# Performance work log

Measured on AMD Instinct MI355X. Metric: run time of the kernel, lower is better.

The kernel has to match this reference:

```python
import jax, jax.numpy as jnp
import numpy as np

B, N, F, H, C, HID = 2, 2048, 64, 4, 32, 128
HIN = H * C  # 128, GAT output width (concat heads)


def setup_inputs() -> dict:
    key = jax.random.key(0)
    ks = jax.random.split(key, 16)
    glorot = jax.nn.initializers.glorot_normal()
    x = jax.random.normal(ks[0], (B, N, F), jnp.float32)
    a = (jax.random.uniform(ks[1], (B, N, N)) < 0.01).astype(jnp.float32)
    a = jnp.maximum(a, jnp.eye(N, dtype=jnp.float32)[None])
    h = jax.random.normal(ks[2], (B, N, HID), jnp.float32)
    # GATConv params (spektral batch mode, concat_heads=True)
    kernel = glorot(ks[3], (F, H, C), jnp.float32)
    attn_self = glorot(ks[4], (H, C), jnp.float32)
    attn_nei = glorot(ks[5], (H, C), jnp.float32)
    bias_gat = jnp.zeros((HIN,), jnp.float32)
    # GRU-style gate params
    b_u = glorot(ks[6], (N, 1), jnp.float32)
    b_r = glorot(ks[7], (N, 1), jnp.float32)
    b_c = glorot(ks[8], (N, 1), jnp.float32)
    W_u = glorot(ks[9], (HID + HIN, HID), jnp.float32)
    W_r = glorot(ks[10], (HID + HIN, HID), jnp.float32)
    W_c = glorot(ks[11], (HID + HIN, HID), jnp.float32)
    # bilinear decoder (p) weight
    R_p = glorot(ks[12], (HID, HID), jnp.float32)
    return {"x": x, "a": a, "h": h, "kernel": kernel, "attn_self": attn_self,
            "attn_nei": attn_nei, "bias_gat": bias_gat, "b_u": b_u, "b_r": b_r,
            "b_c": b_c, "W_u": W_u, "W_r": W_r, "W_c": W_c, "R_p": R_p}


def _gat(x, a, kernel, attn_self, attn_nei, bias_gat):
    # x: [B,N,F] -> per-head features xp: [B,N,H,C]
    xp = jnp.einsum('bnf,fhc->bnhc', x, kernel)
    es = jnp.einsum('bnhc,hc->bnh', xp, attn_self)   # target score
    en = jnp.einsum('bnhc,hc->bnh', xp, attn_nei)    # source score
    # e[b,i,j,h] = leakyrelu(es_i + en_j), masked by adjacency
    e = jax.nn.leaky_relu(es[:, :, None, :] + en[:, None, :, :], 0.2)
    e = e + (-1e9) * (1.0 - a)[..., None]
    alpha = jax.nn.softmax(e, axis=2)                # softmax over sources j
    out = jnp.einsum('bijh,bjhc->bihc', alpha, xp)   # aggregate
    return out.reshape(out.shape[0], out.shape[1], -1) + bias_gat  # [B,N,H*C]


def reference(x, a, h, kernel, attn_self, attn_nei, bias_gat,
              b_u, b_r, b_c, W_u, W_r, W_c, R_p):
    conv_u = _gat(x, a, kernel, attn_self, attn_nei, bias_gat)  # [B,N,HIN]
    z = jnp.concatenate([conv_u, h], axis=-1)                    # [B,N,HIN+HID]
    u = jax.nn.sigmoid(b_u + z @ W_u)                            # b_u [N,1] broadcasts
    r = jax.nn.sigmoid(b_r + z @ W_r)
    zc = jnp.concatenate([conv_u, r * h], axis=-1)
    c = jnp.tanh(b_c + zc @ W_c)
    h_prime = u * h + (1.0 - u) * c                              # [B,N,HID]
    A = jnp.einsum('bnh,hk,bmk->bnm', h_prime, R_p, h_prime)     # bilinear decode [B,N,N]
    return A, h_prime
```

## Files before the change

kernel.cpp:

```cpp
#include <hip/hip_runtime.h>
#include <hip/hip_bf16.h>
#include <math.h>

#define NB 2
#define NN 2048
#define FD 64
#define NH 4
#define HIDD 128
#define ROWS_TOT (NB*NN)

#define XP_OFF   0
#define ES_OFF   524288
#define EN_OFF   540672
#define CU_OFF   557056
#define TBF_OFF  1081344
#define HPBF_OFF 1343488
#define WUH_OFF  1605632
#define WUL_OFF  1622016
#define WRH_OFF  1638400
#define WRL_OFF  1654784
#define WCH_OFF  1671168
#define WCL_OFF  1687552
#define RPH_OFF  1703936
#define RPL_OFF  1712128

#define A_ELEMS (NB*NN*NN)

typedef __attribute__((ext_vector_type(8))) short bf16x8;
typedef __attribute__((ext_vector_type(8))) unsigned short ushort8;
typedef __attribute__((ext_vector_type(4))) unsigned short ushort4v;
typedef __attribute__((ext_vector_type(4))) float f32x4;

#define MFMA_BF16(a,b,c) __builtin_amdgcn_mfma_f32_16x16x32_bf16((a),(b),(c),0,0,0)

static __device__ inline unsigned short f2bf(float x) {
  __hip_bfloat16 b = __float2bfloat16(x);
  unsigned short u; __builtin_memcpy(&u, &b, 2); return u;
}
static __device__ inline float bf2f(unsigned short u) {
  __hip_bfloat16 b; __builtin_memcpy(&b, &u, 2); return __bfloat162float(b);
}
static __device__ inline void split2(float x, unsigned short& hi, unsigned short& lo) {
  hi = f2bf(x);
  lo = f2bf(x - bf2f(hi));
}

__global__ __launch_bounds__(256) void k0_prep(
    const float* __restrict__ Wu, const float* __restrict__ Wr,
    const float* __restrict__ Wc, const float* __restrict__ Rp,
    unsigned short* __restrict__ wuh, unsigned short* __restrict__ wul,
    unsigned short* __restrict__ wrh, unsigned short* __restrict__ wrl,
    unsigned short* __restrict__ wch, unsigned short* __restrict__ wcl,
    unsigned short* __restrict__ rph, unsigned short* __restrict__ rpl)
{
  const int gid = blockIdx.x*256 + threadIdx.x;
  if (gid < 98304) {
    const int which = gid >> 15;
    const int loc = gid & 32767;
    const int e  = loc & 7;
    const int ln = (loc >> 3) & 63;
    const int ks = (loc >> 9) & 7;
    const int jt = loc >> 12;
    const int j = jt*16 + (ln & 15);
    const int k = ks*32 + ((ln >> 4) << 3) + e;
    const float* W = which == 0 ? Wu : (which == 1 ? Wr : Wc);
    unsigned short* oh = which == 0 ? wuh : (which == 1 ? wrh : wch);
    unsigned short* ol = which == 0 ? wul : (which == 1 ? wrl : wcl);
    unsigned short h, l; split2(W[k*128 + j], h, l);
    oh[loc] = h; ol[loc] = l;
  } else if (gid < 114688) {
    const int loc = gid - 98304;
    const int e  = loc & 7;
    const int ln = (loc >> 3) & 63;
    const int ks = (loc >> 9) & 3;
    const int jt = loc >> 11;
    const int j = jt*16 + (ln & 15);
    const int k = ks*32 + ((ln >> 4) << 3) + e;
    unsigned short h, l; split2(Rp[k*128 + j], h, l);
    rph[loc] = h; rpl[loc] = l;
  }
}

__global__ __launch_bounds__(256) void k1_xp(
    const float* __restrict__ x, const float* __restrict__ kern,
    const float* __restrict__ as_, const float* __restrict__ an_,
    float* __restrict__ xp, float* __restrict__ es, float* __restrict__ en)
{
  __shared__ float xr[8][FD];
  const int t = threadIdx.x;
  const int row0 = blockIdx.x * 8;
  for (int idx = t; idx < 8*FD; idx += 256)
    xr[idx >> 6][idx & 63] = x[(size_t)row0*FD + idx];
  __syncthreads();
  const int c4 = (t & 31) * 4;
  const int rq = t >> 5;
  const float4 asv = *(const float4*)(as_ + c4);
  const float4 anv = *(const float4*)(an_ + c4);
  float4 acc = make_float4(0.f, 0.f, 0.f, 0.f);
  for (int f = 0; f < FD; ++f) {
    const float4 kv = *(const float4*)(kern + f*128 + c4);
    const float xv = xr[rq][f];
    acc.x = fmaf(xv, kv.x, acc.x);
    acc.y = fmaf(xv, kv.y, acc.y);
    acc.z = fmaf(xv, kv.z, acc.z);
    acc.w = fmaf(xv, kv.w, acc.w);
  }
  const int grow = row0 + rq;
  *(float4*)(xp + (size_t)grow*128 + c4) = acc;
  float s  = acc.x*asv.x + acc.y*asv.y + acc.z*asv.z + acc.w*asv.w;
  float n_ = acc.x*anv.x + acc.y*anv.y + acc.z*anv.z + acc.w*anv.w;
#pragma unroll
  for (int mk = 4; mk >= 1; mk >>= 1) {
    s  += __shfl_xor(s,  mk, 64);
    n_ += __shfl_xor(n_, mk, 64);
  }
  if ((t & 7) == 0) {
    const int h = (t & 31) >> 3;
    es[grow*NH + h] = s; en[grow*NH + h] = n_;
  }
}

__global__ __launch_bounds__(256) void k2_attn(
    const float* __restrict__ a, const float* __restrict__ xp,
    const float* __restrict__ es, const float* __restrict__ en,
    const float* __restrict__ bias, float* __restrict__ cu)
{
  __shared__ unsigned short sidx[4][NN];
  __shared__ float swl[4][64][NH];
  const int t = threadIdx.x;
  const int ln = t & 63, wv = t >> 6;
  const int row = blockIdx.x * 4 + wv;
  const int b = row >> 11;
  const float4 esi = *(const float4*)(es + (size_t)row*NH);

  int deg = 0;
  const float4* arow4 = (const float4*)(a + (size_t)row*NN);
#pragma unroll
  for (int cch = 0; cch < 8; ++cch) {
    const float4 v = arow4[cch*64 + ln];
    const int j0 = cch*256 + ln*4;
    const float vv[4] = {v.x, v.y, v.z, v.w};
#pragma unroll
    for (int q = 0; q < 4; ++q) {
      const unsigned long long m = __ballot(vv[q] > 0.5f);
      if (vv[q] > 0.5f) {
        const int pos = deg + (int)__popcll(m & ((1ull << ln) - 1ull));
        sidx[wv][pos] = (unsigned short)(j0 + q);
      }
      deg += (int)__popcll(m);
    }
  }

  const int col0 = ln, col1 = ln + 64;
  const int h0 = ln >> 5;
  float m0=-1e30f, m1=-1e30f, m2=-1e30f, m3=-1e30f;
  float s0=0.f, s1=0.f, s2=0.f, s3=0.f;
  float acc0=0.f, acc1=0.f;
  for (int base = 0; base < deg; base += 64) {
    const int rem = min(64, deg - base);
    float t0=-1e30f, t1=-1e30f, t2=-1e30f, t3=-1e30f;
    if (ln < rem) {
      const int j = sidx[wv][base + ln];
      const float4 e4 = *(const float4*)(en + (size_t)(b*NN + j)*NH);
      t0 = esi.x + e4.x; t0 = t0 > 0.f ? t0 : 0.2f*t0;
      t1 = esi.y + e4.y; t1 = t1 > 0.f ? t1 : 0.2f*t1;
      t2 = esi.z + e4.z; t2 = t2 > 0.f ? t2 : 0.2f*t2;
      t3 = esi.w + e4.w; t3 = t3 > 0.f ? t3 : 0.2f*t3;
    }
    float c0=t0, c1=t1, c2=t2, c3=t3;
#pragma unroll
    for (int mk = 32; mk >= 1; mk >>= 1) {
      c0 = fmaxf(c0, __shfl_xor(c0, mk));
      c1 = fmaxf(c1, __shfl_xor(c1, mk));
      c2 = fmaxf(c2, __shfl_xor(c2, mk));
      c3 = fmaxf(c3, __shfl_xor(c3, mk));
    }
    const float nm0 = fmaxf(m0,c0), nm1 = fmaxf(m1,c1);
    const float nm2 = fmaxf(m2,c2), nm3 = fmaxf(m3,c3);
    const float r0 = expf(m0-nm0), r1 = expf(m1-nm1);
    const float r2 = expf(m2-nm2), r3 = expf(m3-nm3);
    s0 *= r0; s1 *= r1; s2 *= r2; s3 *= r3;
    float w0=0.f, w1=0.f, w2=0.f, w3=0.f;
    if (ln < rem) {
      w0 = expf(t0-nm0); w1 = expf(t1-nm1);
      w2 = expf(t2-nm2); w3 = expf(t3-nm3);
    }
    float u0=w0, u1=w1, u2=w2, u3=w3;
#pragma unroll
    for (int mk = 32; mk >= 1; mk >>= 1) {
      u0 += __shfl_xor(u0, mk);
      u1 += __shfl_xor(u1, mk);
      u2 += __shfl_xor(u2, mk);
      u3 += __shfl_xor(u3, mk);
    }
    s0 += u0; s1 += u1; s2 += u2; s3 += u3;
    acc0 *= (h0 ? r1 : r0);
    acc1 *= (h0 ? r3 : r2);
    swl[wv][ln][0] = w0; swl[wv][ln][1] = w1;
    swl[wv][ln][2] = w2; swl[wv][ln][3] = w3;
#pragma unroll 4
    for (int k = 0; k < rem; ++k) {
      const int j = sidx[wv][base + k];
      const float* xr = xp + (size_t)(b*NN + j)*128;
      acc0 = fmaf(swl[wv][k][h0],     xr[col0], acc0);
      acc1 = fmaf(swl[wv][k][2 + h0], xr[col1], acc1);
    }
    m0=nm0; m1=nm1; m2=nm2; m3=nm3;
  }
  const float den0 = h0 ? s1 : s0;
  const float den1 = h0 ? s3 : s2;
  cu[(size_t)row*128 + col0] = acc0/den0 + bias[col0];
  cu[(size_t)row*128 + col1] = acc1/den1 + bias[col1];
}

__global__ __launch_bounds__(512) void k3_mfma(
    const float* __restrict__ cu_, const float* __restrict__ hin,
    const float* __restrict__ bu, const float* __restrict__ br,
    const float* __restrict__ bc,
    const unsigned short* __restrict__ wuh, const unsigned short* __restrict__ wul,
    const unsigned short* __restrict__ wrh, const unsigned short* __restrict__ wrl,
    const unsigned short* __restrict__ wch, const unsigned short* __restrict__ wcl,
    const unsigned short* __restrict__ rph, const unsigned short* __restrict__ rpl,
    float* __restrict__ hp_out,
    __hip_bfloat16* __restrict__ hp_bf, __hip_bfloat16* __restrict__ t_bf)
{
  __shared__ __align__(16) char zH[16*512];
  __shared__ __align__(16) char zL[16*512];
  __shared__ __align__(16) char rhH[16*256];
  __shared__ __align__(16) char rhL[16*256];
  __shared__ __align__(16) char hpH[16*256];
  __shared__ __align__(16) char hpLo[16*256];
  const int t = threadIdx.x;
  const int row0 = blockIdx.x * 16;

#pragma unroll
  for (int i = 0; i < 2; ++i) {
    const int q = t + 512*i;
    const int r = q >> 6;
    const int c = (q & 63) * 4;
    float4 v;
    if (c < 128) v = *(const float4*)(cu_ + (size_t)(row0+r)*128 + c);
    else         v = *(const float4*)(hin + (size_t)(row0+r)*128 + (c-128));
    unsigned short hx, lx, hy, ly, hz, lz, hw, lw;
    split2(v.x, hx, lx); split2(v.y, hy, ly);
    split2(v.z, hz, lz); split2(v.w, hw, lw);
    ushort4v h4; h4[0]=hx; h4[1]=hy; h4[2]=hz; h4[3]=hw;
    ushort4v l4; l4[0]=lx; l4[1]=ly; l4[2]=lz; l4[3]=lw;
    const int byte = (c*2) ^ ((r & 7) << 4);
    *(ushort4v*)(zH + r*512 + byte) = h4;
    *(ushort4v*)(zL + r*512 + byte) = l4;
  }
  __syncthreads();

  const int ln = t & 63, wv = t >> 6;
  const int lr = ln & 15, kid = ln >> 4;
  const int sw = (lr & 7) << 4;
  const int colg = wv*16 + lr;
  const f32x4 zero = {0.f, 0.f, 0.f, 0.f};
  const bf16x8* wuhF = (const bf16x8*)wuh;
  const bf16x8* wulF = (const bf16x8*)wul;
  const bf16x8* wrhF = (const bf16x8*)wrh;
  const bf16x8* wrlF = (const bf16x8*)wrl;
  const bf16x8* wchF = (const bf16x8*)wch;
  const bf16x8* wclF = (const bf16x8*)wcl;
  const bf16x8* rphF = (const bf16x8*)rph;
  const bf16x8* rplF = (const bf16x8*)rpl;

  f32x4 accU = zero, accR = zero;
#pragma unroll
  for (int ks = 0; ks < 8; ++ks) {
    const int kb = ks*64 + kid*16;
    const bf16x8 ah = *(const bf16x8*)(zH + lr*512 + (kb ^ sw));
    const bf16x8 al = *(const bf16x8*)(zL + lr*512 + (kb ^ sw));
    const int fb = (wv*8 + ks)*64 + ln;
    const bf16x8 buH = wuhF[fb];
    const bf16x8 buL = wulF[fb];
    const bf16x8 brH = wrhF[fb];
    const bf16x8 brL = wrlF[fb];
    accU = MFMA_BF16(ah, buH, accU);
    accU = MFMA_BF16(ah, buL, accU);
    accU = MFMA_BF16(al, buH, accU);
    accR = MFMA_BF16(ah, brH, accR);
    accR = MFMA_BF16(ah, brL, accR);
    accR = MFMA_BF16(al, brH, accR);
  }

  float hval[4], uval[4];
#pragma unroll
  for (int reg = 0; reg < 4; ++reg) {
    const int row16 = kid*4 + reg;
    const int grow = row0 + row16;
    const int nrow = grow & (NN-1);
    const float h_ = hin[(size_t)grow*128 + colg];
    const float uv = 1.f/(1.f + expf(-(bu[nrow] + accU[reg])));
    const float rv = 1.f/(1.f + expf(-(br[nrow] + accR[reg])));
    hval[reg] = h_; uval[reg] = uv;
    unsigned short hs, ls; split2(rv * h_, hs, ls);
    const int byte = (colg*2) ^ ((row16 & 7) << 4);
    *(unsigned short*)(rhH + row16*256 + byte) = hs;
    *(unsigned short*)(rhL + row16*256 + byte) = ls;
  }
  __syncthreads();

  f32x4 accC = zero;
#pragma unroll
  for (int ks = 0; ks < 8; ++ks) {
    const int kb = ks*64 + kid*16;
    bf16x8 ah, al;
    if (ks < 4) {
      ah = *(const bf16x8*)(zH + lr*512 + (kb ^ sw));
      al = *(const bf16x8*)(zL + lr*512 + (kb ^ sw));
    } else {
      const int kb2 = (ks-4)*64 + kid*16;
      ah = *(const bf16x8*)(rhH + lr*256 + (kb2 ^ sw));
      al = *(const bf16x8*)(rhL + lr*256 + (kb2 ^ sw));
    }
    const int fb = (wv*8 + ks)*64 + ln;
    const bf16x8 bH = wchF[fb];
    const bf16x8 bL = wclF[fb];
    accC = MFMA_BF16(ah, bH, accC);
    accC = MFMA_BF16(ah, bL, accC);
    accC = MFMA_BF16(al, bH, accC);
  }

#pragma unroll
  for (int reg = 0; reg < 4; ++reg) {
    const int row16 = kid*4 + reg;
    const int grow = row0 + row16;
    const int nrow = grow & (NN-1);
    const float cc = tanhf(bc[nrow] + accC[reg]);
    const float uv = uval[reg];
    const float hpv = uv*hval[reg] + (1.f - uv)*cc;
    hp_out[(size_t)grow*128 + colg] = hpv;
    hp_bf[(size_t)grow*128 + colg] = __float2bfloat16(hpv);
    unsigned short hs, ls; split2(hpv, hs, ls);
    const int byte = (colg*2) ^ ((row16 & 7) << 4);
    *(unsigned short*)(hpH  + row16*256 + byte) = hs;
    *(unsigned short*)(hpLo + row16*256 + byte) = ls;
  }
  __syncthreads();

  f32x4 accT = zero;
#pragma unroll
  for (int ks = 0; ks < 4; ++ks) {
    const int kb = ks*64 + kid*16;
    const bf16x8 ah = *(const bf16x8*)(hpH  + lr*256 + (kb ^ sw));
    const bf16x8 al = *(const bf16x8*)(hpLo + lr*256 + (kb ^ sw));
    const int fb = (wv*4 + ks)*64 + ln;
    const bf16x8 bH = rphF[fb];
    const bf16x8 bL = rplF[fb];
    accT = MFMA_BF16(ah, bH, accT);
    accT = MFMA_BF16(ah, bL, accT);
    accT = MFMA_BF16(al, bH, accT);
  }
#pragma unroll
  for (int reg = 0; reg < 4; ++reg) {
    const int grow = row0 + kid*4 + reg;
    t_bf[(size_t)grow*128 + colg] = __float2bfloat16(accT[reg]);
  }
}

__global__ __launch_bounds__(256) void k4b_dec(
    const __hip_bfloat16* __restrict__ t_bf,
    const __hip_bfloat16* __restrict__ hp_bf,
    float* __restrict__ A)
{
  __shared__ __align__(16) char smem[128*132*4];
  char* Alds = smem;
  char* Blds = smem + 32768;
  float* Cst = (float*)smem;
  const int t = threadIdx.x;
  const int ln = t & 63, wv = t >> 6;
  const int b = blockIdx.z;
  const int i0 = blockIdx.y * 128, j0 = blockIdx.x * 128;

  {
    const int sub = ln >> 4;
    const int cb  = (ln & 15) * 16;
#pragma unroll
    for (int q = 0; q < 8; ++q) {
      const int chunk = wv*8 + q;
      const int row = chunk*4 + sub;
      const int scb = cb ^ ((row & 7) << 4);
      const ushort8 va = *(const ushort8*)
          ((const char*)(t_bf + ((size_t)(b*NN) + i0 + row)*128) + cb);
      *(ushort8*)(Alds + row*256 + scb) = va;
      const ushort8 vb = *(const ushort8*)
          ((const char*)(hp_bf + ((size_t)(b*NN) + j0 + row)*128) + cb);
      *(ushort8*)(Blds + row*256 + scb) = vb;
    }
  }
  __syncthreads();

  const int wr = wv >> 1, wc = wv & 1;
  const int lrow = ln & 15;
  const int kid  = ln >> 4;
  f32x4 acc[4][4];
  const f32x4 zero = {0.f, 0.f, 0.f, 0.f};
#pragma unroll
  for (int m = 0; m < 4; ++m)
#pragma unroll
    for (int n = 0; n < 4; ++n) acc[m][n] = zero;

#pragma unroll
  for (int ks = 0; ks < 4; ++ks) {
    const int kb = ks*64 + kid*16;
    bf16x8 af[4], bfr[4];
#pragma unroll
    for (int m = 0; m < 4; ++m) {
      const int arow = wr*64 + m*16 + lrow;
      af[m] = *(const bf16x8*)(Alds + arow*256 + (kb ^ ((arow & 7) << 4)));
      const int brow = wc*64 + m*16 + lrow;
      bfr[m] = *(const bf16x8*)(Blds + brow*256 + (kb ^ ((brow & 7) << 4)));
    }
#pragma unroll
    for (int m = 0; m < 4; ++m)
#pragma unroll
      for (int n = 0; n < 4; ++n)
        acc[m][n] = MFMA_BF16(af[m], bfr[n], acc[m][n]);
  }
  __syncthreads();

#pragma unroll
  for (int m = 0; m < 4; ++m) {
    const int crow = wr*64 + m*16 + kid*4;
#pragma unroll
    for (int n = 0; n < 4; ++n) {
      const int ccol = wc*64 + n*16 + lrow;
#pragma unroll
      for (int r = 0; r < 4; ++r)
        Cst[(crow + r)*132 + ccol] = acc[m][n][r];
    }
  }
  __syncthreads();

#pragma unroll
  for (int p = 0; p < 16; ++p) {
    const int row = p*8 + (t >> 5);
    const int c4  = (t & 31) * 4;
    const float4 v = *(const float4*)&Cst[row*132 + c4];
    *(float4*)(A + ((size_t)b*NN + i0 + row)*NN + j0 + c4) = v;
  }
}

extern "C" void kernel_launch(void* const* d_in, const int* in_sizes, int n_in,
                              void* d_out, int out_size, void* d_ws, size_t ws_size,
                              hipStream_t stream)
{
  const float* x    = (const float*)d_in[0];
  const float* a    = (const float*)d_in[1];
  const float* h    = (const float*)d_in[2];
  const float* kern = (const float*)d_in[3];
  const float* as_  = (const float*)d_in[4];
  const float* an_  = (const float*)d_in[5];
  const float* bias = (const float*)d_in[6];
  const float* bu   = (const float*)d_in[7];
  const float* br   = (const float*)d_in[8];
  const float* bc   = (const float*)d_in[9];
  const float* Wu   = (const float*)d_in[10];
  const float* Wr   = (const float*)d_in[11];
  const float* Wc   = (const float*)d_in[12];
  const float* Rp   = (const float*)d_in[13];
  (void)in_sizes; (void)n_in; (void)out_size; (void)ws_size;

  float* ws = (float*)d_ws;
  float* xp = ws + XP_OFF;
  float* es = ws + ES_OFF;
  float* en = ws + EN_OFF;
  float* cu = ws + CU_OFF;
  __hip_bfloat16* t_bf  = (__hip_bfloat16*)(ws + TBF_OFF);
  __hip_bfloat16* hp_bf = (__hip_bfloat16*)(ws + HPBF_OFF);
  unsigned short* wuh = (unsigned short*)(ws + WUH_OFF);
  unsigned short* wul = (unsigned short*)(ws + WUL_OFF);
  unsigned short* wrh = (unsigned short*)(ws + WRH_OFF);
  unsigned short* wrl = (unsigned short*)(ws + WRL_OFF);
  unsigned short* wch = (unsigned short*)(ws + WCH_OFF);
  unsigned short* wcl = (unsigned short*)(ws + WCL_OFF);
  unsigned short* rph = (unsigned short*)(ws + RPH_OFF);
  unsigned short* rpl = (unsigned short*)(ws + RPL_OFF);

  float* A  = (float*)d_out;
  float* hp = (float*)d_out + A_ELEMS;

  hipLaunchKernelGGL(k0_prep, dim3(448), dim3(256), 0, stream,
                     Wu, Wr, Wc, Rp, wuh, wul, wrh, wrl, wch, wcl, rph, rpl);
  hipLaunchKernelGGL(k1_xp,   dim3(ROWS_TOT/8), dim3(256), 0, stream,
                     x, kern, as_, an_, xp, es, en);
  hipLaunchKernelGGL(k2_attn, dim3(ROWS_TOT/4), dim3(256), 0, stream,
                     a, xp, es, en, bias, cu);
  hipLaunchKernelGGL(k3_mfma, dim3(ROWS_TOT/16), dim3(512), 0, stream,
                     cu, h, bu, br, bc, wuh, wul, wrh, wrl, wch, wcl, rph, rpl,
                     hp, hp_bf, t_bf);
  hipLaunchKernelGGL(k4b_dec, dim3(NN/128, NN/128, NB), dim3(256), 0, stream,
                     t_bf, hp_bf, A);
}
```

Before: 143.5 us.

## Merge weight prep into xp kernel and split k3 GEMM K-dimension across waves

Merges the weight split/swizzle prep kernel with the xp projection kernel into one launch by block-index dispatch, removing one kernel launch and its gap. The GRU/decoder MFMA kernel now uses 1024 threads, with two wave halves each taking half the K range and combining partial sums through shared memory. This doubles the waves per block for more latency hiding, at the cost of extra LDS traffic and barriers, and leaves half the waves idle during the epilogues. It also adds an unroll pragma on the xp inner loop.

```diff
diff --git a/kernel.cpp b/kernel.cpp
--- a/kernel.cpp
+++ b/kernel.cpp
@@ -45,50 +45,49 @@
   lo = f2bf(x - bf2f(hi));
 }
 
-__global__ __launch_bounds__(256) void k0_prep(
+__global__ __launch_bounds__(256) void k01_prep_xp(
     const float* __restrict__ Wu, const float* __restrict__ Wr,
     const float* __restrict__ Wc, const float* __restrict__ Rp,
     unsigned short* __restrict__ wuh, unsigned short* __restrict__ wul,
     unsigned short* __restrict__ wrh, unsigned short* __restrict__ wrl,
     unsigned short* __restrict__ wch, unsigned short* __restrict__ wcl,
-    unsigned short* __restrict__ rph, unsigned short* __restrict__ rpl)
-{
-  const int gid = blockIdx.x*256 + threadIdx.x;
-  if (gid < 98304) {
-    const int which = gid >> 15;
-    const int loc = gid & 32767;
-    const int e  = loc & 7;
-    const int ln = (loc >> 3) & 63;
-    const int ks = (loc >> 9) & 7;
-    const int jt = loc >> 12;
-    const int j = jt*16 + (ln & 15);
-    const int k = ks*32 + ((ln >> 4) << 3) + e;
-    const float* W = which == 0 ? Wu : (which == 1 ? Wr : Wc);
-    unsigned short* oh = which == 0 ? wuh : (which == 1 ? wrh : wch);
-    unsigned short* ol = which == 0 ? wul : (which == 1 ? wrl : wcl);
-    unsigned short h, l; split2(W[k*128 + j], h, l);
-    oh[loc] = h; ol[loc] = l;
-  } else if (gid < 114688) {
-    const int loc = gid - 98304;
-    const int e  = loc & 7;
-    const int ln = (loc >> 3) & 63;
-    const int ks = (loc >> 9) & 3;
-    const int jt = loc >> 11;
-    const int j = jt*16 + (ln & 15);
-    const int k = ks*32 + ((ln >> 4) << 3) + e;
-    unsigned short h, l; split2(Rp[k*128 + j], h, l);
-    rph[loc] = h; rpl[loc] = l;
-  }
-}
-
-__global__ __launch_bounds__(256) void k1_xp(
+    unsigned short* __restrict__ rph, unsigned short* __restrict__ rpl,
     const float* __restrict__ x, const float* __restrict__ kern,
     const float* __restrict__ as_, const float* __restrict__ an_,
     float* __restrict__ xp, float* __restrict__ es, float* __restrict__ en)
 {
   __shared__ float xr[8][FD];
   const int t = threadIdx.x;
-  const int row0 = blockIdx.x * 8;
+  if (blockIdx.x < 448) {
+    const int gid = blockIdx.x*256 + t;
+    if (gid < 98304) {
+      const int which = gid >> 15;
+      const int loc = gid & 32767;
+      const int e  = loc & 7;
+      const int ln = (loc >> 3) & 63;
+      const int ks = (loc >> 9) & 7;
+      const int jt = loc >> 12;
+      const int j = jt*16 + (ln & 15);
+      const int k = ks*32 + ((ln >> 4) << 3) + e;
+      const float* W = which == 0 ? Wu : (which == 1 ? Wr : Wc);
+      unsigned short* oh = which == 0 ? wuh : (which == 1 ? wrh : wch);
+      unsigned short* ol = which == 0 ? wul : (which == 1 ? wrl : wcl);
+      unsigned short h, l; split2(W[k*128 + j], h, l);
+      oh[loc] = h; ol[loc] = l;
+    } else if (gid < 114688) {
+      const int loc = gid - 98304;
+      const int e  = loc & 7;
+      const int ln = (loc >> 3) & 63;
+      const int ks = (loc >> 9) & 3;
+      const int jt = loc >> 11;
+      const int j = jt*16 + (ln & 15);
+      const int k = ks*32 + ((ln >> 4) << 3) + e;
+      unsigned short h, l; split2(Rp[k*128 + j], h, l);
+      rph[loc] = h; rpl[loc] = l;
+    }
+    return;
+  }
+  const int row0 = (blockIdx.x - 448) * 8;
   for (int idx = t; idx < 8*FD; idx += 256)
     xr[idx >> 6][idx & 63] = x[(size_t)row0*FD + idx];
   __syncthreads();
@@ -97,6 +96,7 @@
   const float4 asv = *(const float4*)(as_ + c4);
   const float4 anv = *(const float4*)(an_ + c4);
   float4 acc = make_float4(0.f, 0.f, 0.f, 0.f);
+#pragma unroll 8
   for (int f = 0; f < FD; ++f) {
     const float4 kv = *(const float4*)(kern + f*128 + c4);
     const float xv = xr[rq][f];
@@ -213,7 +213,7 @@
   cu[(size_t)row*128 + col1] = acc1/den1 + bias[col1];
 }
 
-__global__ __launch_bounds__(512) void k3_mfma(
+__global__ __launch_bounds__(1024) void k3_mfma(
     const float* __restrict__ cu_, const float* __restrict__ hin,
     const float* __restrict__ bu, const float* __restrict__ br,
     const float* __restrict__ bc,
@@ -226,16 +226,18 @@
 {
   __shared__ __align__(16) char zH[16*512];
   __shared__ __align__(16) char zL[16*512];
-  __shared__ __align__(16) char rhH[16*256];
-  __shared__ __align__(16) char rhL[16*256];
-  __shared__ __align__(16) char hpH[16*256];
-  __shared__ __align__(16) char hpLo[16*256];
+  __shared__ __align__(16) char red[32768];
+  char* rhH  = red;
+  char* rhL  = red + 4096;
+  char* hpH  = red + 8192;
+  char* hpLo = red + 12288;
+  float* redA = (float*)red;
+  float* redB = (float*)(red + 16384);
   const int t = threadIdx.x;
   const int row0 = blockIdx.x * 16;
 
-#pragma unroll
-  for (int i = 0; i < 2; ++i) {
-    const int q = t + 512*i;
+  {
+    const int q = t;
     const int r = q >> 6;
     const int c = (q & 63) * 4;
     float4 v;
@@ -252,10 +254,11 @@
   }
   __syncthreads();
 
-  const int ln = t & 63, wv = t >> 6;
+  const int ln = t & 63, w = t >> 6;
+  const int jt = w & 7, half = w >> 3;
   const int lr = ln & 15, kid = ln >> 4;
   const int sw = (lr & 7) << 4;
-  const int colg = wv*16 + lr;
+  const int colg = jt*16 + lr;
   const f32x4 zero = {0.f, 0.f, 0.f, 0.f};
   const bf16x8* wuhF = (const bf16x8*)wuh;
   const bf16x8* wulF = (const bf16x8*)wul;
@@ -268,11 +271,12 @@
 
   f32x4 accU = zero, accR = zero;
 #pragma unroll
-  for (int ks = 0; ks < 8; ++ks) {
+  for (int i = 0; i < 4; ++i) {
+    const int ks = half*4 + i;
     const int kb = ks*64 + kid*16;
     const bf16x8 ah = *(const bf16x8*)(zH + lr*512 + (kb ^ sw));
     const bf16x8 al = *(const bf16x8*)(zL + lr*512 + (kb ^ sw));
-    const int fb = (wv*8 + ks)*64 + ln;
+    const int fb = (jt*8 + ks)*64 + ln;
     const bf16x8 buH = wuhF[fb];
     const bf16x8 buL = wulF[fb];
     const bf16x8 brH = wrhF[fb];
@@ -284,79 +288,98 @@
     accR = MFMA_BF16(ah, brL, accR);
     accR = MFMA_BF16(al, brH, accR);
   }
+  *(f32x4*)(redA + w*256 + ln*4) = accU;
+  *(f32x4*)(redB + w*256 + ln*4) = accR;
+  __syncthreads();
 
   float hval[4], uval[4];
-#pragma unroll
-  for (int reg = 0; reg < 4; ++reg) {
-    const int row16 = kid*4 + reg;
-    const int grow = row0 + row16;
-    const int nrow = grow & (NN-1);
-    const float h_ = hin[(size_t)grow*128 + colg];
-    const float uv = 1.f/(1.f + expf(-(bu[nrow] + accU[reg])));
-    const float rv = 1.f/(1.f + expf(-(br[nrow] + accR[reg])));
-    hval[reg] = h_; uval[reg] = uv;
-    unsigned short hs, ls; split2(rv * h_, hs, ls);
-    const int byte = (colg*2) ^ ((row16 & 7) << 4);
-    *(unsigned short*)(rhH + row16*256 + byte) = hs;
-    *(unsigned short*)(rhL + row16*256 + byte) = ls;
+  if (half == 0) {
+    accU += *(const f32x4*)(redA + (w+8)*256 + ln*4);
+    accR += *(const f32x4*)(redB + (w+8)*256 + ln*4);
+#pragma unroll
+    for (int reg = 0; reg < 4; ++reg) {
+      const int row16 = kid*4 + reg;
+      const int grow = row0 + row16;
+      const int nrow = grow & (NN-1);
+      const float h_ = hin[(size_t)grow*128 + colg];
+      const float uv = 1.f/(1.f + expf(-(bu[nrow] + accU[reg])));
+      const float rv = 1.f/(1.f + expf(-(br[nrow] + accR[reg])));
+      hval[reg] = h_; uval[reg] = uv;
+      unsigned short hs, ls; split2(rv * h_, hs, ls);
+      const int byte = (colg*2) ^ ((row16 & 7) << 4);
+      *(unsigned short*)(rhH + row16*256 + byte) = hs;
+      *(unsigned short*)(rhL + row16*256 + byte) = ls;
+    }
   }
   __syncthreads();
 
   f32x4 accC = zero;
 #pragma unroll
-  for (int ks = 0; ks < 8; ++ks) {
-    const int kb = ks*64 + kid*16;
+  for (int i = 0; i < 4; ++i) {
+    const int kb = i*64 + kid*16;
     bf16x8 ah, al;
-    if (ks < 4) {
+    if (half == 0) {
       ah = *(const bf16x8*)(zH + lr*512 + (kb ^ sw));
       al = *(const bf16x8*)(zL + lr*512 + (kb ^ sw));
     } else {
-      const int kb2 = (ks-4)*64 + kid*16;
-      ah = *(const bf16x8*)(rhH + lr*256 + (kb2 ^ sw));
-      al = *(const bf16x8*)(rhL + lr*256 + (kb2 ^ sw));
-    }
-    const int fb = (wv*8 + ks)*64 + ln;
+      ah = *(const bf16x8*)(rhH + lr*256 + (kb ^ sw));
+      al = *(const bf16x8*)(rhL + lr*256 + (kb ^ sw));
+    }
+    const int ks = half*4 + i;
+    const int fb = (jt*8 + ks)*64 + ln;
     const bf16x8 bH = wchF[fb];
     const bf16x8 bL = wclF[fb];
     accC = MFMA_BF16(ah, bH, accC);
     accC = MFMA_BF16(ah, bL, accC);
     accC = MFMA_BF16(al, bH, accC);
   }
-
-#pragma unroll
-  for (int reg = 0; reg < 4; ++reg) {
-    const int row16 = kid*4 + reg;
-    const int grow = row0 + row16;
-    const int nrow = grow & (NN-1);
-    const float cc = tanhf(bc[nrow] + accC[reg]);
-    const float uv = uval[reg];
-    const float hpv = uv*hval[reg] + (1.f - uv)*cc;
-    hp_out[(size_t)grow*128 + colg] = hpv;
-    hp_bf[(size_t)grow*128 + colg] = __float2bfloat16(hpv);
-    unsigned short hs, ls; split2(hpv, hs, ls);
-    const int byte = (colg*2) ^ ((row16 & 7) << 4);
-    *(unsigned short*)(hpH  + row16*256 + byte) = hs;
-    *(unsigned short*)(hpLo + row16*256 + byte) = ls;
+  *(f32x4*)(redB + w*256 + ln*4) = accC;
+  __syncthreads();
+
+  if (half == 0) {
+    accC += *(const f32x4*)(redB + (w+8)*256 + ln*4);
+#pragma unroll
+    for (int reg = 0; reg < 4; ++reg) {
+      const int row16 = kid*4 + reg;
+      const int grow = row0 + row16;
+      const int nrow = grow & (NN-1);
+      const float cc = tanhf(bc[nrow] + accC[reg]);
+      const float uv = uval[reg];
+      const float hpv = uv*hval[reg] + (1.f - uv)*cc;
+      hp_out[(size_t)grow*128 + colg] = hpv;
+      hp_bf[(size_t)grow*128 + colg] = __float2bfloat16(hpv);
+      unsigned short hs, ls; split2(hpv, hs, ls);
+      const int byte = (colg*2) ^ ((row16 & 7) << 4);
+      *(unsigned short*)(hpH  + row16*256 + byte) = hs;
+      *(unsigned short*)(hpLo + row16*256 + byte) = ls;
+    }
   }
   __syncthreads();
 
   f32x4 accT = zero;
 #pragma unroll
-  for (int ks = 0; ks < 4; ++ks) {
+  for (int i = 0; i < 2; ++i) {
+    const int ks = half*2 + i;
     const int kb = ks*64 + kid*16;
     const bf16x8 ah = *(const bf16x8*)(hpH  + lr*256 + (kb ^ sw));
     const bf16x8 al = *(const bf16x8*)(hpLo + lr*256 + (kb ^ sw));
-    const int fb = (wv*4 + ks)*64 + ln;
+    const int fb = (jt*4 + ks)*64 + ln;
     const bf16x8 bH = rphF[fb];
     const bf16x8 bL = rplF[fb];
     accT = MFMA_BF16(ah, bH, accT);
     accT = MFMA_BF16(ah, bL, accT);
     accT = MFMA_BF16(al, bH, accT);
   }
-#pragma unroll
-  for (int reg = 0; reg < 4; ++reg) {
-    const int grow = row0 + kid*4 + reg;
-    t_bf[(size_t)grow*128 + colg] = __float2bfloat16(accT[reg]);
+  *(f32x4*)(redB + w*256 + ln*4) = accT;
+  __syncthreads();
+
+  if (half == 0) {
+    accT += *(const f32x4*)(redB + (w+8)*256 + ln*4);
+#pragma unroll
+    for (int reg = 0; reg < 4; ++reg) {
+      const int grow = row0 + kid*4 + reg;
+      t_bf[(size_t)grow*128 + colg] = __float2bfloat16(accT[reg]);
+    }
   }
 }
 
@@ -482,13 +505,12 @@
   float* A  = (float*)d_out;
   float* hp = (float*)d_out + A_ELEMS;
 
-  hipLaunchKernelGGL(k0_prep, dim3(448), dim3(256), 0, stream,
-                     Wu, Wr, Wc, Rp, wuh, wul, wrh, wrl, wch, wcl, rph, rpl);
-  hipLaunchKernelGGL(k1_xp,   dim3(ROWS_TOT/8), dim3(256), 0, stream,
+  hipLaunchKernelGGL(k01_prep_xp, dim3(448 + ROWS_TOT/8), dim3(256), 0, stream,
+                     Wu, Wr, Wc, Rp, wuh, wul, wrh, wrl, wch, wcl, rph, rpl,
                      x, kern, as_, an_, xp, es, en);
   hipLaunchKernelGGL(k2_attn, dim3(ROWS_TOT/4), dim3(256), 0, stream,
                      a, xp, es, en, bias, cu);
-  hipLaunchKernelGGL(k3_mfma, dim3(ROWS_TOT/16), dim3(512), 0, stream,
+  hipLaunchKernelGGL(k3_mfma, dim3(ROWS_TOT/16), dim3(1024), 0, stream,
                      cu, h, bu, br, bc, wuh, wul, wrh, wrl, wch, wcl, rph, rpl,
                      hp, hp_bf, t_bf);
   hipLaunchKernelGGL(k4b_dec, dim3(NN/128, NN/128, NB), dim3(256), 0, stream,
```

After: 143.0 us. About the same (-0.4%).
